# Kernel tuning notes

Measured on AMD Instinct MI355X. Metric: run time of the kernel, lower is better.

Reference implementation:

```python
import jax, jax.numpy as jnp
import numpy as np

TEMPERATURE = 8.0  # sqrt(d_k)

def setup_inputs() -> dict:
    key = jax.random.key(0)
    ks = jax.random.split(key, 9)
    B, H, LQ, LK, D = 8, 8, 1024, 1024, 64
    s = 0.125  # keep projection chain well-scaled (1/sqrt(D))
    return {
        "q":    jax.random.normal(ks[0], (B, LQ, H, D), jnp.float32),
        "W_A":  jax.random.normal(ks[1], (H, D, D), jnp.float32) * s,
        "W_B":  jax.random.normal(ks[2], (H, D, D), jnp.float32) * s,
        "W_At": jax.random.normal(ks[3], (H, D, D), jnp.float32) * s,
        "W_Bt": jax.random.normal(ks[4], (H, D, D), jnp.float32) * s,
        "W_av": jax.random.normal(ks[5], (H, D, D), jnp.float32) * s,
        "W_bv": jax.random.normal(ks[6], (H, D, D), jnp.float32) * s,
        "qt":   jax.random.normal(ks[7], (B, H, D, LK), jnp.float32),
        "v":    jax.random.normal(ks[8], (B, LK, H, D), jnp.float32),
        "d_k":  64,
    }

def reference(q, W_A, W_B, W_At, W_Bt, W_av, W_bv, qt, v, d_k):
    # attn = einsum('kabc,bcd,bdi,bim,bmj,kbjn->kban') / temperature
    # Fold the per-head square projection chain first (optimal contraction order):
    # W[b] = W_A[b] @ W_B[b] @ W_Bt[b] @ W_At[b]  -> [H, D, D] (axes b,c,j)
    W = jnp.einsum('bcd,bdi,bim,bmj->bcj', W_A, W_B, W_Bt, W_At)
    # scores: [batch, heads, len_q, len_k]
    attn = jnp.einsum('kabc,bcj,kbjn->kban', q, W, qt) / TEMPERATURE
    attn = jax.nn.softmax(attn, axis=-1)  # dropout is identity in eval mode
    # output = einsum('kbjm,kmbn,bna,bac->kbjc'); fold W_av @ W_bv -> [H, D, D]
    Wv = jnp.einsum('bna,bac->bnc', W_av, W_bv)
    output = jnp.einsum('kbjm,kmbn,bnc->kbjc', attn, v, Wv)
    return (output, attn)
```

## Files before the change

### kernel.cpp

```cpp
#include <hip/hip_runtime.h>
#include <hip/hip_bf16.h>

#define NB 8
#define NH 8
#define LQ 1024
#define LK 1024
#define DD 64
#define EC 0.18033688011112042f
#define OUT0_SIZE (8ull*8*1024*64)

typedef __bf16 bf16x8 __attribute__((ext_vector_type(8)));
typedef __bf16 bf16x4 __attribute__((ext_vector_type(4)));
typedef float  f32x4  __attribute__((ext_vector_type(4)));
typedef unsigned int u32x2 __attribute__((ext_vector_type(2)));

static __device__ __forceinline__ __bf16 f2b(float f) {
    unsigned u = __builtin_bit_cast(unsigned, f);
    unsigned r = (u + 0x7fffu + ((u >> 16) & 1u)) >> 16;
    return __builtin_bit_cast(__bf16, (unsigned short)r);
}
static __device__ __forceinline__ unsigned bpack(float a, float b) {
    return (unsigned)__builtin_bit_cast(unsigned short, f2b(a))
         | ((unsigned)__builtin_bit_cast(unsigned short, f2b(b)) << 16);
}
static __device__ __forceinline__ void gload16(const void* g, void* l) {
    __builtin_amdgcn_global_load_lds(
        (const __attribute__((address_space(1))) void*)g,
        (__attribute__((address_space(3))) void*)l, 16, 0, 0);
}

__global__ __launch_bounds__(256) void fold_pairs(
        const float* __restrict__ pWA, const float* __restrict__ pWB,
        const float* __restrict__ pWBt, const float* __restrict__ pWAt,
        const float* __restrict__ pWav, const float* __restrict__ pWbv,
        float* __restrict__ P1, float* __restrict__ P2, float* __restrict__ Wv) {
    __shared__ float AT[64*68];
    __shared__ float Bl[64*64];
    const int h = blockIdx.x / 3;
    const int which = blockIdx.x - h*3;
    const int t = threadIdx.x;
    const float *A, *B; float* C;
    if (which == 0)      { A = pWA  + h*4096; B = pWB  + h*4096; C = P1 + h*4096; }
    else if (which == 1) { A = pWBt + h*4096; B = pWAt + h*4096; C = P2 + h*4096; }
    else                 { A = pWav + h*4096; B = pWbv + h*4096; C = Wv + h*4096; }

    for (int i = t; i < 4096; i += 256) {
        int r = i >> 6, c = i & 63;
        AT[c*68 + r] = A[i];
        Bl[i] = B[i];
    }
    __syncthreads();
    const int r0 = (t >> 4) * 4, j0 = (t & 15) * 4;
    float acc[4][4] = {};
    #pragma unroll 8
    for (int k = 0; k < 64; ++k) {
        f32x4 a = *(const f32x4*)&AT[k*68 + r0];
        f32x4 b = *(const f32x4*)&Bl[k*64 + j0];
        #pragma unroll
        for (int i = 0; i < 4; ++i)
            #pragma unroll
            for (int j = 0; j < 4; ++j) acc[i][j] += a[i] * b[j];
    }
    #pragma unroll
    for (int i = 0; i < 4; ++i) {
        f32x4 o = { acc[i][0], acc[i][1], acc[i][2], acc[i][3] };
        *(f32x4*)&C[(r0 + i)*64 + j0] = o;
    }
}

__global__ __launch_bounds__(256) void fold_final(
        const float* __restrict__ P1, const float* __restrict__ P2,
        float* __restrict__ Wout) {
    __shared__ float AT[64*68];
    __shared__ float Bl[64*64];
    const int h = blockIdx.x;
    const int t = threadIdx.x;
    for (int i = t; i < 4096; i += 256) {
        int r = i >> 6, c = i & 63;
        AT[c*68 + r] = P1[h*4096 + i];
        Bl[i] = P2[h*4096 + i];
    }
    __syncthreads();
    const int r0 = (t >> 4) * 4, j0 = (t & 15) * 4;
    float acc[4][4] = {};
    #pragma unroll 8
    for (int k = 0; k < 64; ++k) {
        f32x4 a = *(const f32x4*)&AT[k*68 + r0];
        f32x4 b = *(const f32x4*)&Bl[k*64 + j0];
        #pragma unroll
        for (int i = 0; i < 4; ++i)
            #pragma unroll
            for (int j = 0; j < 4; ++j) acc[i][j] += a[i] * b[j];
    }
    #pragma unroll
    for (int i = 0; i < 4; ++i) {
        f32x4 o = { acc[i][0], acc[i][1], acc[i][2], acc[i][3] };
        *(f32x4*)&Wout[h*4096 + (r0 + i)*64 + j0] = o;
    }
}

__global__ __launch_bounds__(256) void prepass(
        const float* __restrict__ q, const float* __restrict__ W,
        const float* __restrict__ qt, const float* __restrict__ v,
        const float* __restrict__ Wv,
        __bf16* __restrict__ qW, __bf16* __restrict__ qtT,
        __bf16* __restrict__ vWT) {
    __shared__ float smem[8448];
    const int bh = blockIdx.x;
    const int by = blockIdx.y;
    const int batch = bh >> 3, h = bh & 7;
    const int t = threadIdx.x;

    if (by < 16) {
        float* qT = smem;
        float* Wl = smem + 4352;
        const int a0 = by * 64;
        for (int i = t; i < 4096; i += 256) {
            int r = i >> 6, c = i & 63;
            Wl[i] = W[h*4096 + i];
            qT[c*68 + r] = q[(((size_t)batch*LQ + a0 + r)*NH + h)*DD + c];
        }
        __syncthreads();
        const int r0 = (t >> 4) * 4, j0 = (t & 15) * 4;
        float acc[4][4] = {};
        #pragma unroll 8
        for (int c = 0; c < 64; ++c) {
            f32x4 a = *(const f32x4*)&qT[c*68 + r0];
            f32x4 b = *(const f32x4*)&Wl[c*64 + j0];
            #pragma unroll
            for (int i = 0; i < 4; ++i)
                #pragma unroll
                for (int j = 0; j < 4; ++j) acc[i][j] += a[i] * b[j];
        }
        #pragma unroll
        for (int i = 0; i < 4; ++i) {
            bf16x4 o;
            #pragma unroll
            for (int j = 0; j < 4; ++j) o[j] = f2b(acc[i][j]);
            *(bf16x4*)&qW[((size_t)bh*LQ + a0 + r0 + i)*DD + j0] = o;
        }
    } else if (by < 24) {
        float* tile = smem;
        const int n0 = (by - 16) * 128;
        #pragma unroll
        for (int it = 0; it < 8; ++it) {
            int idx = (t + 256*it) * 4;
            int j = idx >> 7, n = idx & 127;
            *(f32x4*)&tile[j*132 + n] = *(const f32x4*)&qt[((size_t)bh*DD + j)*LK + n0 + n];
        }
        __syncthreads();
        const int j0 = (t & 15) * 4;
        #pragma unroll
        for (int it = 0; it < 8; ++it) {
            int n = (t >> 4) + 16*it;
            bf16x4 o;
            #pragma unroll
            for (int i = 0; i < 4; ++i) o[i] = f2b(tile[(j0 + i)*132 + n]);
            *(bf16x4*)&qtT[((size_t)bh*LK + n0 + n)*DD + j0] = o;
        }
    } else {
        float* vT  = smem;
        float* Wvl = smem + 4352;
        const int mb0 = (by - 24) * 64;
        const int mb  = by - 24;
        for (int i = t; i < 4096; i += 256) {
            int r = i >> 6, c = i & 63;
            Wvl[i] = Wv[h*4096 + i];
            vT[c*68 + r] = v[(((size_t)batch*LK + mb0 + r)*NH + h)*DD + c];
        }
        __syncthreads();
        const int c0 = (t >> 4) * 4, m0 = (t & 15) * 4;
        float acc[4][4] = {};
        #pragma unroll 8
        for (int n = 0; n < 64; ++n) {
            f32x4 wv = *(const f32x4*)&Wvl[n*64 + c0];
            f32x4 vv = *(const f32x4*)&vT[n*68 + m0];
            #pragma unroll
            for (int ci = 0; ci < 4; ++ci)
                #pragma unroll
                for (int mi = 0; mi < 4; ++mi) acc[ci][mi] += wv[ci] * vv[mi];
        }
        #pragma unroll
        for (int ci = 0; ci < 4; ++ci) {
            bf16x4 o;
            #pragma unroll
            for (int mi = 0; mi < 4; ++mi) o[mi] = f2b(acc[ci][mi]);
            *(bf16x4*)&vWT[((((size_t)bh*16 + mb)*64) + c0 + ci)*64 + m0] = o;
        }
    }
}

__global__ __launch_bounds__(256) void attn_kernel(
        const __bf16* __restrict__ qW, const __bf16* __restrict__ qtT,
        const __bf16* __restrict__ vWT, float* __restrict__ out) {
    __shared__ __align__(16) char smem[76032];
    __bf16* Kb   = (__bf16*)(smem);
    __bf16* Vb   = (__bf16*)(smem + 32768);
    __bf16* El   = (__bf16*)(smem + 65536);
    float*  rsb  = (float*) (smem + 75776);
    float*  Pt0  = (float*) (smem);
    float*  Obuf = (float*) (smem + 18432);

    const int bid = blockIdx.x;
    const int xcd = bid & 7, s = bid >> 3;
    const int bh  = xcd * 8 + (s >> 5);
    const int a0  = (s & 31) * 32;
    const int t   = threadIdx.x;
    const int w   = t >> 6, l = t & 63;
    const int lg  = l & 15, g = l >> 4;
    const int strip = w & 1, nh = w >> 1;
    const int qbase = a0 + strip * 16;
    const int n0w   = nh * 512;
    const int srow = l >> 3, scol = l & 7;
    const int swz  = scol ^ srow;

    const __bf16* qtb = qtT + (size_t)bh * LK * DD;
    const __bf16* vwb = vWT + (size_t)bh * LK * DD;

    __bf16* Kbw  = Kb + (size_t)nh * 8192;
    __bf16* Vbw  = Vb + (size_t)nh * 8192;
    __bf16* eldw = El + (size_t)w * 16 * 80;

    const bf16x8* qWp = reinterpret_cast<const bf16x8*>(qW + ((size_t)bh*LQ + qbase + lg)*DD);
    bf16x8 bfrag0 = qWp[g];
    bf16x8 bfrag1 = qWp[g + 4];

    const __bf16* gK = qtb + (size_t)(nh*512)*64;
    const __bf16* gV = vwb;

    const int sw0 = (g ^ (lg & 7)) * 8;
    const int sw1 = ((g + 4) ^ (lg & 7)) * 8;

#define STAGE(NC, DB)                                                          \
    if ((w & 1) == 0) {                                                        \
        const __bf16* src = gK + (size_t)((NC)*64 + srow)*64 + swz*8;          \
        __bf16* dst = Kbw + (DB)*4096;                                         \
        _Pragma("unroll")                                                      \
        for (int i = 0; i < 8; ++i)                                            \
            gload16(src + (size_t)i*512, dst + i*512);                         \
    } else {                                                                   \
        const __bf16* src = gV + (size_t)(nh*8 + (NC))*4096 + (size_t)srow*64 + swz*8; \
        __bf16* dst = Vbw + (DB)*4096;                                         \
        _Pragma("unroll")                                                      \
        for (int i = 0; i < 8; ++i)                                            \
            gload16(src + (size_t)i*512, dst + i*512);                         \
    }

    STAGE(0, 0);
    __syncthreads();

    u32x2 ppk[8][4];
    float rsum = 0.f;
    f32x4 oacc[4];
    #pragma unroll
    for (int ct = 0; ct < 4; ++ct) oacc[ct] = f32x4{0.f, 0.f, 0.f, 0.f};

    #pragma unroll
    for (int nc = 0; nc < 8; ++nc) {
        const int db = nc & 1;
        if (nc < 7) { STAGE(nc + 1, db ^ 1); }
        const __bf16* Kcur = Kbw + db*4096;
        f32x4 accs[4];
        #pragma unroll
        for (int sub = 0; sub < 4; ++sub) {
            const __bf16* kr = Kcur + (sub*16 + lg)*64;
            bf16x8 a0 = *(const bf16x8*)&kr[sw0];
            bf16x8 a1 = *(const bf16x8*)&kr[sw1];
            f32x4 acc = {0.f, 0.f, 0.f, 0.f};
            acc = __builtin_amdgcn_mfma_f32_16x16x32_bf16(a0, bfrag0, acc, 0, 0, 0);
            acc = __builtin_amdgcn_mfma_f32_16x16x32_bf16(a1, bfrag1, acc, 0, 0, 0);
            accs[sub] = acc;
        }
        #pragma unroll
        for (int sub = 0; sub < 4; ++sub) {
            float p0 = __builtin_exp2f(accs[sub][0] * EC);
            float p1 = __builtin_exp2f(accs[sub][1] * EC);
            float p2 = __builtin_exp2f(accs[sub][2] * EC);
            float p3 = __builtin_exp2f(accs[sub][3] * EC);
            rsum += (p0 + p1) + (p2 + p3);
            u32x2 pk;
            pk.x = bpack(p0, p1);
            pk.y = bpack(p2, p3);
            ppk[nc][sub] = pk;
            *(u32x2*)&eldw[lg*80 + sub*16 + g*4] = pk;
        }
        const __bf16* er = &eldw[lg*80];
        bf16x8 pf0 = *(const bf16x8*)&er[g*8];
        bf16x8 pf1 = *(const bf16x8*)&er[g*8 + 32];
        const __bf16* Vcur = Vbw + db*4096;
        #pragma unroll
        for (int ct = 0; ct < 4; ++ct) {
            const __bf16* vr = Vcur + (ct*16 + lg)*64;
            bf16x8 v0 = *(const bf16x8*)&vr[sw0];
            bf16x8 v1 = *(const bf16x8*)&vr[sw1];
            oacc[ct] = __builtin_amdgcn_mfma_f32_16x16x32_bf16(v0, pf0, oacc[ct], 0, 0, 0);
            oacc[ct] = __builtin_amdgcn_mfma_f32_16x16x32_bf16(v1, pf1, oacc[ct], 0, 0, 0);
        }
        __syncthreads();
    }

    rsum += __shfl_xor(rsum, 16);
    rsum += __shfl_xor(rsum, 32);
    if (l < 16) rsb[(nh*2 + strip)*16 + l] = rsum;
    __syncthreads();
    const float rinv = 1.0f / (rsb[(0*2 + strip)*16 + lg] + rsb[(1*2 + strip)*16 + lg]);

    #pragma unroll
    for (int ct = 0; ct < 4; ++ct) oacc[ct] *= rinv;

    const int rr = l >> 4, cc = l & 15;
    if (nh == 1) {
        #pragma unroll
        for (int ct = 0; ct < 4; ++ct)
            *(f32x4*)&Obuf[(strip*16 + lg)*72 + ct*16 + g*4] = oacc[ct];
    }
    __syncthreads();
    if (nh == 0) {
        #pragma unroll
        for (int ct = 0; ct < 4; ++ct) {
            f32x4 o = *(const f32x4*)&Obuf[(strip*16 + lg)*72 + ct*16 + g*4];
            o = o + oacc[ct];
            *(f32x4*)&Obuf[(strip*16 + lg)*72 + ct*16 + g*4] = o;
        }
    }
    __syncthreads();
    #pragma unroll
    for (int it = 0; it < 2; ++it) {
        int row = it*16 + w*4 + rr;
        f32x4 o = *(const f32x4*)&Obuf[row*72 + cc*4];
        __builtin_nontemporal_store(o,
            (f32x4*)&out[(((size_t)bh*LQ + a0 + row) << 6) + cc*4]);
    }

    float* ptw = Pt0 + (size_t)w * 16 * 72;
    float* attnb = out + OUT0_SIZE + ((size_t)bh << 20);
    #pragma unroll
    for (int nc = 0; nc < 8; ++nc) {
        const int nbase = n0w + nc*64;
        #pragma unroll
        for (int sub = 0; sub < 4; ++sub) {
            unsigned lo = ppk[nc][sub].x, hi = ppk[nc][sub].y;
            f32x4 ps;
            ps[0] = __builtin_bit_cast(float, lo << 16) * rinv;
            ps[1] = __builtin_bit_cast(float, lo & 0xffff0000u) * rinv;
            ps[2] = __builtin_bit_cast(float, hi << 16) * rinv;
            ps[3] = __builtin_bit_cast(float, hi & 0xffff0000u) * rinv;
            *(f32x4*)&ptw[lg*72 + sub*16 + g*4] = ps;
        }
        #pragma unroll
        for (int it = 0; it < 4; ++it) {
            int row = it*4 + rr;
            f32x4 pp = *(const f32x4*)&ptw[row*72 + cc*4];
            __builtin_nontemporal_store(pp,
                (f32x4*)&attnb[((size_t)(qbase + row) << 10) + nbase + cc*4]);
        }
    }
#undef STAGE
}

extern "C" void kernel_launch(void* const* d_in, const int* in_sizes, int n_in,
                              void* d_out, int out_size, void* d_ws, size_t ws_size,
                              hipStream_t stream) {
    const float* q   = (const float*)d_in[0];
    const float* WA  = (const float*)d_in[1];
    const float* WB  = (const float*)d_in[2];
    const float* WAt = (const float*)d_in[3];
    const float* WBt = (const float*)d_in[4];
    const float* Wav = (const float*)d_in[5];
    const float* Wbv = (const float*)d_in[6];
    const float* qt  = (const float*)d_in[7];
    const float* v   = (const float*)d_in[8];
    float* out = (float*)d_out;

    char* ws = (char*)d_ws;
    float*  W    = (float*)(ws);
    float*  Wv   = (float*)(ws + 131072);
    __bf16* qW   = (__bf16*)(ws + 262144);
    __bf16* qtT  = (__bf16*)(ws + 262144 + 8388608);
    __bf16* vWT  = (__bf16*)(ws + 262144 + 2*8388608);
    float*  P1   = (float*)(ws + 262144);
    float*  P2   = (float*)(ws + 262144 + 131072);

    hipLaunchKernelGGL(fold_pairs, dim3(24), dim3(256), 0, stream,
                       WA, WB, WBt, WAt, Wav, Wbv, P1, P2, Wv);
    hipLaunchKernelGGL(fold_final, dim3(8),  dim3(256), 0, stream, P1, P2, W);
    hipLaunchKernelGGL(prepass,    dim3(64, 40), dim3(256), 0, stream,
                       q, W, qt, v, Wv, qW, qtT, vWT);
    hipLaunchKernelGGL(attn_kernel, dim3(2048), dim3(256), 0, stream,
                       qW, qtT, vWT, out);
}
```

Measured before the change: 108.1 us.

## Split attention into K-pass then V-pass sharing one double-buffered LDS region

The fused loop used to stream K and V tiles together and do QK, softmax and PV per chunk. It now runs two passes. The first streams only K tiles to compute exp scores and row sums. The second streams V tiles and does the PV MFMA while also writing the normalized attention matrix. Because K and V share one double-buffered LDS area, shared memory drops from about 76 KB to about 62 KB, which may allow two blocks per CU and overlaps the attention stores with the V loads and MFMAs. The cost is a second loop with extra barriers, and the per-thread sum is split into four accumulators.

```diff
diff --git a/kernel.cpp b/kernel.cpp
--- a/kernel.cpp
+++ b/kernel.cpp
@@ -193,13 +193,12 @@
 __global__ __launch_bounds__(256) void attn_kernel(
         const __bf16* __restrict__ qW, const __bf16* __restrict__ qtT,
         const __bf16* __restrict__ vWT, float* __restrict__ out) {
-    __shared__ __align__(16) char smem[76032];
-    __bf16* Kb   = (__bf16*)(smem);
-    __bf16* Vb   = (__bf16*)(smem + 32768);
-    __bf16* El   = (__bf16*)(smem + 65536);
-    float*  rsb  = (float*) (smem + 75776);
-    float*  Pt0  = (float*) (smem);
-    float*  Obuf = (float*) (smem + 18432);
+    __shared__ __align__(16) char smem[61696];
+    __bf16* KV   = (__bf16*)(smem);
+    __bf16* El   = (__bf16*)(smem + 32768);
+    float*  Pt0  = (float*) (smem + 43008);
+    float*  rsb  = (float*) (smem + 61440);
+    float*  Obuf = (float*) (smem);
 
     const int bid = blockIdx.x;
     const int xcd = bid & 7, s = bid >> 3;
@@ -217,49 +216,45 @@
     const __bf16* qtb = qtT + (size_t)bh * LK * DD;
     const __bf16* vwb = vWT + (size_t)bh * LK * DD;
 
-    __bf16* Kbw  = Kb + (size_t)nh * 8192;
-    __bf16* Vbw  = Vb + (size_t)nh * 8192;
     __bf16* eldw = El + (size_t)w * 16 * 80;
+    float*  ptw  = Pt0 + (size_t)w * 16 * 72;
 
     const bf16x8* qWp = reinterpret_cast<const bf16x8*>(qW + ((size_t)bh*LQ + qbase + lg)*DD);
     bf16x8 bfrag0 = qWp[g];
     bf16x8 bfrag1 = qWp[g + 4];
 
-    const __bf16* gK = qtb + (size_t)(nh*512)*64;
-    const __bf16* gV = vwb;
-
     const int sw0 = (g ^ (lg & 7)) * 8;
     const int sw1 = ((g + 4) ^ (lg & 7)) * 8;
 
-#define STAGE(NC, DB)                                                          \
-    if ((w & 1) == 0) {                                                        \
-        const __bf16* src = gK + (size_t)((NC)*64 + srow)*64 + swz*8;          \
-        __bf16* dst = Kbw + (DB)*4096;                                         \
+#define STAGE_K(NC, DB)                                                        \
+    {                                                                          \
+        const __bf16* src = qtb + (size_t)(nh*512 + (NC)*64 + strip*32 + srow)*64 + swz*8; \
+        __bf16* dst = KV + nh*8192 + (DB)*4096 + strip*2048;                   \
         _Pragma("unroll")                                                      \
-        for (int i = 0; i < 8; ++i)                                            \
+        for (int i = 0; i < 4; ++i)                                            \
             gload16(src + (size_t)i*512, dst + i*512);                         \
-    } else {                                                                   \
-        const __bf16* src = gV + (size_t)(nh*8 + (NC))*4096 + (size_t)srow*64 + swz*8; \
-        __bf16* dst = Vbw + (DB)*4096;                                         \
+    }
+#define STAGE_V(NC, DB)                                                        \
+    {                                                                          \
+        const __bf16* src = vwb + (size_t)(nh*8 + (NC))*4096 + (size_t)(strip*32 + srow)*64 + swz*8; \
+        __bf16* dst = KV + nh*8192 + (DB)*4096 + strip*2048;                   \
         _Pragma("unroll")                                                      \
-        for (int i = 0; i < 8; ++i)                                            \
+        for (int i = 0; i < 4; ++i)                                            \
             gload16(src + (size_t)i*512, dst + i*512);                         \
     }
 
-    STAGE(0, 0);
+    STAGE_K(0, 0);
     __syncthreads();
 
     u32x2 ppk[8][4];
-    float rsum = 0.f;
-    f32x4 oacc[4];
-    #pragma unroll
-    for (int ct = 0; ct < 4; ++ct) oacc[ct] = f32x4{0.f, 0.f, 0.f, 0.f};
+    float rs0 = 0.f, rs1 = 0.f, rs2 = 0.f, rs3 = 0.f;
 
     #pragma unroll
     for (int nc = 0; nc < 8; ++nc) {
         const int db = nc & 1;
-        if (nc < 7) { STAGE(nc + 1, db ^ 1); }
-        const __bf16* Kcur = Kbw + db*4096;
+        if (nc < 7) { STAGE_K(nc + 1, db ^ 1); }
+        else        { STAGE_V(0, db ^ 1); }
+        const __bf16* Kcur = KV + nh*8192 + db*4096;
         f32x4 accs[4];
         #pragma unroll
         for (int sub = 0; sub < 4; ++sub) {
@@ -277,65 +272,32 @@
             float p1 = __builtin_exp2f(accs[sub][1] * EC);
             float p2 = __builtin_exp2f(accs[sub][2] * EC);
             float p3 = __builtin_exp2f(accs[sub][3] * EC);
-            rsum += (p0 + p1) + (p2 + p3);
+            rs0 += p0; rs1 += p1; rs2 += p2; rs3 += p3;
             u32x2 pk;
             pk.x = bpack(p0, p1);
             pk.y = bpack(p2, p3);
             ppk[nc][sub] = pk;
-            *(u32x2*)&eldw[lg*80 + sub*16 + g*4] = pk;
-        }
-        const __bf16* er = &eldw[lg*80];
-        bf16x8 pf0 = *(const bf16x8*)&er[g*8];
-        bf16x8 pf1 = *(const bf16x8*)&er[g*8 + 32];
-        const __bf16* Vcur = Vbw + db*4096;
-        #pragma unroll
-        for (int ct = 0; ct < 4; ++ct) {
-            const __bf16* vr = Vcur + (ct*16 + lg)*64;
-            bf16x8 v0 = *(const bf16x8*)&vr[sw0];
-            bf16x8 v1 = *(const bf16x8*)&vr[sw1];
-            oacc[ct] = __builtin_amdgcn_mfma_f32_16x16x32_bf16(v0, pf0, oacc[ct], 0, 0, 0);
-            oacc[ct] = __builtin_amdgcn_mfma_f32_16x16x32_bf16(v1, pf1, oacc[ct], 0, 0, 0);
-        }
-        __syncthreads();
-    }
-
+        }
+        __syncthreads();
+    }
+
+    float rsum = (rs0 + rs1) + (rs2 + rs3);
     rsum += __shfl_xor(rsum, 16);
     rsum += __shfl_xor(rsum, 32);
     if (l < 16) rsb[(nh*2 + strip)*16 + l] = rsum;
     __syncthreads();
     const float rinv = 1.0f / (rsb[(0*2 + strip)*16 + lg] + rsb[(1*2 + strip)*16 + lg]);
 
-    #pragma unroll
-    for (int ct = 0; ct < 4; ++ct) oacc[ct] *= rinv;
-
     const int rr = l >> 4, cc = l & 15;
-    if (nh == 1) {
-        #pragma unroll
-        for (int ct = 0; ct < 4; ++ct)
-            *(f32x4*)&Obuf[(strip*16 + lg)*72 + ct*16 + g*4] = oacc[ct];
-    }
-    __syncthreads();
-    if (nh == 0) {
-        #pragma unroll
-        for (int ct = 0; ct < 4; ++ct) {
-            f32x4 o = *(const f32x4*)&Obuf[(strip*16 + lg)*72 + ct*16 + g*4];
-            o = o + oacc[ct];
-            *(f32x4*)&Obuf[(strip*16 + lg)*72 + ct*16 + g*4] = o;
-        }
-    }
-    __syncthreads();
-    #pragma unroll
-    for (int it = 0; it < 2; ++it) {
-        int row = it*16 + w*4 + rr;
-        f32x4 o = *(const f32x4*)&Obuf[row*72 + cc*4];
-        __builtin_nontemporal_store(o,
-            (f32x4*)&out[(((size_t)bh*LQ + a0 + row) << 6) + cc*4]);
-    }
-
-    float* ptw = Pt0 + (size_t)w * 16 * 72;
     float* attnb = out + OUT0_SIZE + ((size_t)bh << 20);
+    f32x4 oacc[4];
+    #pragma unroll
+    for (int ct = 0; ct < 4; ++ct) oacc[ct] = f32x4{0.f, 0.f, 0.f, 0.f};
+
     #pragma unroll
     for (int nc = 0; nc < 8; ++nc) {
+        const int db = nc & 1;
+        if (nc < 7) { STAGE_V(nc + 1, db ^ 1); }
         const int nbase = n0w + nc*64;
         #pragma unroll
         for (int sub = 0; sub < 4; ++sub) {
@@ -346,6 +308,7 @@
             ps[2] = __builtin_bit_cast(float, hi << 16) * rinv;
             ps[3] = __builtin_bit_cast(float, hi & 0xffff0000u) * rinv;
             *(f32x4*)&ptw[lg*72 + sub*16 + g*4] = ps;
+            *(u32x2*)&eldw[lg*80 + sub*16 + g*4] = ppk[nc][sub];
         }
         #pragma unroll
         for (int it = 0; it < 4; ++it) {
@@ -354,8 +317,48 @@
             __builtin_nontemporal_store(pp,
                 (f32x4*)&attnb[((size_t)(qbase + row) << 10) + nbase + cc*4]);
         }
-    }
-#undef STAGE
+        const __bf16* er = &eldw[lg*80];
+        bf16x8 pf0 = *(const bf16x8*)&er[g*8];
+        bf16x8 pf1 = *(const bf16x8*)&er[g*8 + 32];
+        const __bf16* Vcur = KV + nh*8192 + db*4096;
+        #pragma unroll
+        for (int ct = 0; ct < 4; ++ct) {
+            const __bf16* vr = Vcur + (ct*16 + lg)*64;
+            bf16x8 v0 = *(const bf16x8*)&vr[sw0];
+            bf16x8 v1 = *(const bf16x8*)&vr[sw1];
+            oacc[ct] = __builtin_amdgcn_mfma_f32_16x16x32_bf16(v0, pf0, oacc[ct], 0, 0, 0);
+            oacc[ct] = __builtin_amdgcn_mfma_f32_16x16x32_bf16(v1, pf1, oacc[ct], 0, 0, 0);
+        }
+        __syncthreads();
+    }
+
+    #pragma unroll
+    for (int ct = 0; ct < 4; ++ct) oacc[ct] *= rinv;
+
+    if (nh == 1) {
+        #pragma unroll
+        for (int ct = 0; ct < 4; ++ct)
+            *(f32x4*)&Obuf[(strip*16 + lg)*72 + ct*16 + g*4] = oacc[ct];
+    }
+    __syncthreads();
+    if (nh == 0) {
+        #pragma unroll
+        for (int ct = 0; ct < 4; ++ct) {
+            f32x4 o = *(const f32x4*)&Obuf[(strip*16 + lg)*72 + ct*16 + g*4];
+            o = o + oacc[ct];
+            *(f32x4*)&Obuf[(strip*16 + lg)*72 + ct*16 + g*4] = o;
+        }
+    }
+    __syncthreads();
+    #pragma unroll
+    for (int it = 0; it < 2; ++it) {
+        int row = it*16 + w*4 + rr;
+        f32x4 o = *(const f32x4*)&Obuf[row*72 + cc*4];
+        __builtin_nontemporal_store(o,
+            (f32x4*)&out[(((size_t)bh*LQ + a0 + row) << 6) + cc*4]);
+    }
+#undef STAGE_K
+#undef STAGE_V
 }
 
 extern "C" void kernel_launch(void* const* d_in, const int* in_sizes, int n_in,
```

Result: slower. 132.4 us (+22.5%).

## Process two query tiles per block and overlap first tile's attn stores with second compute

Applied to the files above, without the earlier changes.

Each block now handles two 32-row query tiles sequentially and the grid is halved. The first tile's normalized attention probabilities are streamed to global memory interleaved with the second tile's K/V staging and MFMA work, which hides store latency behind compute. The output for the first tile is reduced through a separate shared region and written directly from registers. This doubles the packed-probability register arrays, which raises register pressure and may lower occupancy. The attention stores for the first tile are now uncoalesced per-lane 16-byte writes instead of going through the shared-memory transpose.

```diff
diff --git a/kernel.cpp b/kernel.cpp
--- a/kernel.cpp
+++ b/kernel.cpp
@@ -198,18 +198,22 @@
     __bf16* Vb   = (__bf16*)(smem + 32768);
     __bf16* El   = (__bf16*)(smem + 65536);
     float*  rsb  = (float*) (smem + 75776);
+    float*  OA   = (float*) (smem + 65536);
     float*  Pt0  = (float*) (smem);
     float*  Obuf = (float*) (smem + 18432);
 
     const int bid = blockIdx.x;
     const int xcd = bid & 7, s = bid >> 3;
-    const int bh  = xcd * 8 + (s >> 5);
-    const int a0  = (s & 31) * 32;
+    const int bh  = xcd * 8 + (s >> 4);
+    const int apair = s & 15;
+    const int a0A = apair * 64;
+    const int a0B = a0A + 32;
     const int t   = threadIdx.x;
     const int w   = t >> 6, l = t & 63;
     const int lg  = l & 15, g = l >> 4;
     const int strip = w & 1, nh = w >> 1;
-    const int qbase = a0 + strip * 16;
+    const int qbaseA = a0A + strip * 16;
+    const int qbaseB = a0B + strip * 16;
     const int n0w   = nh * 512;
     const int srow = l >> 3, scol = l & 7;
     const int swz  = scol ^ srow;
@@ -221,9 +225,12 @@
     __bf16* Vbw  = Vb + (size_t)nh * 8192;
     __bf16* eldw = El + (size_t)w * 16 * 80;
 
-    const bf16x8* qWp = reinterpret_cast<const bf16x8*>(qW + ((size_t)bh*LQ + qbase + lg)*DD);
-    bf16x8 bfrag0 = qWp[g];
-    bf16x8 bfrag1 = qWp[g + 4];
+    const bf16x8* qWpA = reinterpret_cast<const bf16x8*>(qW + ((size_t)bh*LQ + qbaseA + lg)*DD);
+    bf16x8 bfragA0 = qWpA[g];
+    bf16x8 bfragA1 = qWpA[g + 4];
+    const bf16x8* qWpB = reinterpret_cast<const bf16x8*>(qW + ((size_t)bh*LQ + qbaseB + lg)*DD);
+    bf16x8 bfragB0 = qWpB[g];
+    bf16x8 bfragB1 = qWpB[g + 4];
 
     const __bf16* gK = qtb + (size_t)(nh*512)*64;
     const __bf16* gV = vwb;
@@ -249,7 +256,7 @@
     STAGE(0, 0);
     __syncthreads();
 
-    u32x2 ppk[8][4];
+    u32x2 ppkA[8][4], ppkB[8][4];
     float rsum = 0.f;
     f32x4 oacc[4];
     #pragma unroll
@@ -267,8 +274,8 @@
             bf16x8 a0 = *(const bf16x8*)&kr[sw0];
             bf16x8 a1 = *(const bf16x8*)&kr[sw1];
             f32x4 acc = {0.f, 0.f, 0.f, 0.f};
-            acc = __builtin_amdgcn_mfma_f32_16x16x32_bf16(a0, bfrag0, acc, 0, 0, 0);
-            acc = __builtin_amdgcn_mfma_f32_16x16x32_bf16(a1, bfrag1, acc, 0, 0, 0);
+            acc = __builtin_amdgcn_mfma_f32_16x16x32_bf16(a0, bfragA0, acc, 0, 0, 0);
+            acc = __builtin_amdgcn_mfma_f32_16x16x32_bf16(a1, bfragA1, acc, 0, 0, 0);
             accs[sub] = acc;
         }
         #pragma unroll
@@ -281,7 +288,7 @@
             u32x2 pk;
             pk.x = bpack(p0, p1);
             pk.y = bpack(p2, p3);
-            ppk[nc][sub] = pk;
+            ppkA[nc][sub] = pk;
             *(u32x2*)&eldw[lg*80 + sub*16 + g*4] = pk;
         }
         const __bf16* er = &eldw[lg*80];
@@ -299,14 +306,101 @@
         __syncthreads();
     }
 
+    STAGE(0, 0);
+
     rsum += __shfl_xor(rsum, 16);
     rsum += __shfl_xor(rsum, 32);
     if (l < 16) rsb[(nh*2 + strip)*16 + l] = rsum;
     __syncthreads();
-    const float rinv = 1.0f / (rsb[(0*2 + strip)*16 + lg] + rsb[(1*2 + strip)*16 + lg]);
-
-    #pragma unroll
-    for (int ct = 0; ct < 4; ++ct) oacc[ct] *= rinv;
+    const float rinvA = 1.0f / (rsb[(0*2 + strip)*16 + lg] + rsb[(1*2 + strip)*16 + lg]);
+
+    #pragma unroll
+    for (int ct = 0; ct < 4; ++ct) oacc[ct] *= rinvA;
+    if (nh == 1) {
+        #pragma unroll
+        for (int ct = 0; ct < 4; ++ct)
+            *(f32x4*)&OA[(strip*16 + lg)*68 + ct*16 + g*4] = oacc[ct];
+    }
+    __syncthreads();
+    if (nh == 0) {
+        #pragma unroll
+        for (int ct = 0; ct < 4; ++ct) {
+            f32x4 o = *(const f32x4*)&OA[(strip*16 + lg)*68 + ct*16 + g*4];
+            o = o + oacc[ct];
+            __builtin_nontemporal_store(o,
+                (f32x4*)&out[(((size_t)bh*LQ + qbaseA + lg) << 6) + ct*16 + g*4]);
+        }
+    }
+    __syncthreads();
+
+    rsum = 0.f;
+    #pragma unroll
+    for (int ct = 0; ct < 4; ++ct) oacc[ct] = f32x4{0.f, 0.f, 0.f, 0.f};
+    float* attnb = out + OUT0_SIZE + ((size_t)bh << 20);
+
+    #pragma unroll
+    for (int nc = 0; nc < 8; ++nc) {
+        const int db = nc & 1;
+        if (nc < 7) { STAGE(nc + 1, db ^ 1); }
+        #pragma unroll
+        for (int sub = 0; sub < 4; ++sub) {
+            unsigned lo = ppkA[nc][sub].x, hi = ppkA[nc][sub].y;
+            f32x4 ps;
+            ps[0] = __builtin_bit_cast(float, lo << 16) * rinvA;
+            ps[1] = __builtin_bit_cast(float, lo & 0xffff0000u) * rinvA;
+            ps[2] = __builtin_bit_cast(float, hi << 16) * rinvA;
+            ps[3] = __builtin_bit_cast(float, hi & 0xffff0000u) * rinvA;
+            __builtin_nontemporal_store(ps,
+                (f32x4*)&attnb[((size_t)(qbaseA + lg) << 10) + n0w + nc*64 + sub*16 + g*4]);
+        }
+        const __bf16* Kcur = Kbw + db*4096;
+        f32x4 accs[4];
+        #pragma unroll
+        for (int sub = 0; sub < 4; ++sub) {
+            const __bf16* kr = Kcur + (sub*16 + lg)*64;
+            bf16x8 a0 = *(const bf16x8*)&kr[sw0];
+            bf16x8 a1 = *(const bf16x8*)&kr[sw1];
+            f32x4 acc = {0.f, 0.f, 0.f, 0.f};
+            acc = __builtin_amdgcn_mfma_f32_16x16x32_bf16(a0, bfragB0, acc, 0, 0, 0);
+            acc = __builtin_amdgcn_mfma_f32_16x16x32_bf16(a1, bfragB1, acc, 0, 0, 0);
+            accs[sub] = acc;
+        }
+        #pragma unroll
+        for (int sub = 0; sub < 4; ++sub) {
+            float p0 = __builtin_exp2f(accs[sub][0] * EC);
+            float p1 = __builtin_exp2f(accs[sub][1] * EC);
+            float p2 = __builtin_exp2f(accs[sub][2] * EC);
+            float p3 = __builtin_exp2f(accs[sub][3] * EC);
+            rsum += (p0 + p1) + (p2 + p3);
+            u32x2 pk;
+            pk.x = bpack(p0, p1);
+            pk.y = bpack(p2, p3);
+            ppkB[nc][sub] = pk;
+            *(u32x2*)&eldw[lg*80 + sub*16 + g*4] = pk;
+        }
+        const __bf16* er = &eldw[lg*80];
+        bf16x8 pf0 = *(const bf16x8*)&er[g*8];
+        bf16x8 pf1 = *(const bf16x8*)&er[g*8 + 32];
+        const __bf16* Vcur = Vbw + db*4096;
+        #pragma unroll
+        for (int ct = 0; ct < 4; ++ct) {
+            const __bf16* vr = Vcur + (ct*16 + lg)*64;
+            bf16x8 v0 = *(const bf16x8*)&vr[sw0];
+            bf16x8 v1 = *(const bf16x8*)&vr[sw1];
+            oacc[ct] = __builtin_amdgcn_mfma_f32_16x16x32_bf16(v0, pf0, oacc[ct], 0, 0, 0);
+            oacc[ct] = __builtin_amdgcn_mfma_f32_16x16x32_bf16(v1, pf1, oacc[ct], 0, 0, 0);
+        }
+        __syncthreads();
+    }
+
+    rsum += __shfl_xor(rsum, 16);
+    rsum += __shfl_xor(rsum, 32);
+    if (l < 16) rsb[(nh*2 + strip)*16 + l] = rsum;
+    __syncthreads();
+    const float rinvB = 1.0f / (rsb[(0*2 + strip)*16 + lg] + rsb[(1*2 + strip)*16 + lg]);
+
+    #pragma unroll
+    for (int ct = 0; ct < 4; ++ct) oacc[ct] *= rinvB;
 
     const int rr = l >> 4, cc = l & 15;
     if (nh == 1) {
@@ -329,22 +423,21 @@
         int row = it*16 + w*4 + rr;
         f32x4 o = *(const f32x4*)&Obuf[row*72 + cc*4];
         __builtin_nontemporal_store(o,
-            (f32x4*)&out[(((size_t)bh*LQ + a0 + row) << 6) + cc*4]);
+            (f32x4*)&out[(((size_t)bh*LQ + a0B + row) << 6) + cc*4]);
     }
 
     float* ptw = Pt0 + (size_t)w * 16 * 72;
-    float* attnb = out + OUT0_SIZE + ((size_t)bh << 20);
     #pragma unroll
     for (int nc = 0; nc < 8; ++nc) {
         const int nbase = n0w + nc*64;
         #pragma unroll
         for (int sub = 0; sub < 4; ++sub) {
-            unsigned lo = ppk[nc][sub].x, hi = ppk[nc][sub].y;
+            unsigned lo = ppkB[nc][sub].x, hi = ppkB[nc][sub].y;
             f32x4 ps;
-            ps[0] = __builtin_bit_cast(float, lo << 16) * rinv;
-            ps[1] = __builtin_bit_cast(float, lo & 0xffff0000u) * rinv;
-            ps[2] = __builtin_bit_cast(float, hi << 16) * rinv;
-            ps[3] = __builtin_bit_cast(float, hi & 0xffff0000u) * rinv;
+            ps[0] = __builtin_bit_cast(float, lo << 16) * rinvB;
+            ps[1] = __builtin_bit_cast(float, lo & 0xffff0000u) * rinvB;
+            ps[2] = __builtin_bit_cast(float, hi << 16) * rinvB;
+            ps[3] = __builtin_bit_cast(float, hi & 0xffff0000u) * rinvB;
             *(f32x4*)&ptw[lg*72 + sub*16 + g*4] = ps;
         }
         #pragma unroll
@@ -352,7 +445,7 @@
             int row = it*4 + rr;
             f32x4 pp = *(const f32x4*)&ptw[row*72 + cc*4];
             __builtin_nontemporal_store(pp,
-                (f32x4*)&attnb[((size_t)(qbase + row) << 10) + nbase + cc*4]);
+                (f32x4*)&attnb[((size_t)(qbaseB + row) << 10) + nbase + cc*4]);
         }
     }
 #undef STAGE
@@ -386,6 +479,6 @@
     hipLaunchKernelGGL(fold_final, dim3(8),  dim3(256), 0, stream, P1, P2, W);
     hipLaunchKernelGGL(prepass,    dim3(64, 40), dim3(256), 0, stream,
                        q, W, qt, v, Wv, qW, qtT, vWT);
-    hipLaunchKernelGGL(attn_kernel, dim3(2048), dim3(256), 0, stream,
+    hipLaunchKernelGGL(attn_kernel, dim3(1024), dim3(256), 0, stream,
                        qW, qtT, vWT, out);
 }
```

Result: slower. 120.4 us (+11.5%).
